# Optimization experiments

Measured on AMD Instinct MI355X. Metric: run time of the kernel, lower is better.

Reference implementation:

```python
import jax, jax.numpy as jnp
import numpy as np

K = 20  # n_neighbors
SLOPE = 0.2

def _act(h):
    return jax.nn.leaky_relu(h, negative_slope=SLOPE)

def _knn_indices(pts):
    # pts: (B, 3, N). Returns (B, N, K) indices of nearest neighbors (by -||xi-xj||^2).
    sq = jnp.sum(pts * pts, axis=1)                      # (B, N)
    inner = jnp.einsum('bcn,bcm->bnm', pts, pts)         # (B, N, N)
    neg_dist = 2.0 * inner - sq[:, :, None] - sq[:, None, :]
    _, idx = jax.lax.top_k(neg_dist, K)                  # (B, N, K)
    return idx

def _gather_neighbors(feats, idx):
    # feats: (B, N, C), idx: (B, N, K) -> (B, N, K, C)
    return jax.vmap(lambda f, i: f[i])(feats, idx)

def setup_inputs() -> dict:
    key = jax.random.key(0)
    ks = jax.random.split(key, 7)
    B, N = 16, 2048
    dims = [64, 64, 128, 256]
    s = 0.05
    inp = {
        'x':  jax.random.normal(ks[0], (B, N, 3), jnp.float32),
        'W0': jax.random.normal(ks[1], (dims[0], 6), jnp.float32) * s,
        'b0': jnp.zeros((dims[0],), jnp.float32),
        'W1': jax.random.normal(ks[2], (dims[1], dims[0]), jnp.float32) * s,
        'b1': jnp.zeros((dims[1],), jnp.float32),
        'W2': jax.random.normal(ks[3], (dims[2], dims[1]), jnp.float32) * s,
        'b2': jnp.zeros((dims[2],), jnp.float32),
        'W3': jax.random.normal(ks[4], (dims[3], dims[2]), jnp.float32) * s,
        'b3': jnp.zeros((dims[3],), jnp.float32),
        'Wf': jax.random.normal(ks[5], (1024, sum(dims)), jnp.float32) * s,
        'bf': jnp.zeros((1024,), jnp.float32),
    }
    return inp

def reference(x, W0, b0, W1, b1, W2, b2, W3, b3, Wf, bf):
    # x: (B, N, 3)
    pts = jnp.swapaxes(x, 1, 2)                          # (B, 3, N)
    idx = _knn_indices(pts)                              # (B, N, K)

    # get_graph_features: edge feats = [neighbor - center, center], (B, N, K, 6)
    neigh = _gather_neighbors(x, idx)                    # (B, N, K, 3)
    center = jnp.broadcast_to(x[:, :, None, :], neigh.shape)
    edge = jnp.concatenate([neigh - center, center], axis=-1)

    # EdgeConv (1x1 conv) + act, then max over neighbors
    h = _act(jnp.einsum('bnkc,oc->bnko', edge, W0) + b0)  # (B, N, K, 64)
    feat = jnp.max(h, axis=2)                             # (B, N, 64)

    xs = [feat]
    for W, b in ((W1, b1), (W2, b2), (W3, b3)):
        # graph max pooling over the fixed kNN graph
        pooled = jnp.max(_gather_neighbors(feat, idx), axis=2)  # (B, N, C)
        feat = _act(jnp.einsum('bnc,oc->bno', pooled, W) + b)
        xs.append(feat)

    cat = jnp.concatenate(xs, axis=-1)                    # (B, N, 512)
    out = _act(jnp.einsum('bnc,oc->bno', cat, Wf) + bf)   # (B, N, 1024)
    return jnp.max(out, axis=1)                           # (B, 1024)
```

## Files before the change

### kernel.cpp

```cpp
#include <hip/hip_runtime.h>

#define K_NN 20
#define NEG_INF (-__builtin_inff())

constexpr int BB   = 16;
constexpr int NN   = 2048;
constexpr int CATC = 512;
constexpr int ROW_G = BB * NN;

typedef short bf16x8 __attribute__((ext_vector_type(8)));
typedef float f32x4  __attribute__((ext_vector_type(4)));

__device__ __forceinline__ unsigned short f2bf_rn(float f) {
  unsigned int u = __float_as_uint(f);
  unsigned int r = u + 0x7FFFu + ((u >> 16) & 1u);
  return (unsigned short)(r >> 16);
}
__device__ __forceinline__ float bf2f(unsigned short h) {
  return __uint_as_float((unsigned int)h << 16);
}
__device__ __forceinline__ void split_store(float v, unsigned short* ph, unsigned short* pl) {
  const unsigned short h = f2bf_rn(v);
  *ph = h;
  *pl = f2bf_rn(v - bf2f(h));
}
__device__ __forceinline__ float join_hl(unsigned short h, unsigned short l) {
  return bf2f(h) + bf2f(l);
}

__device__ __forceinline__ int mbcnt(unsigned long long mask) {
  return __builtin_amdgcn_mbcnt_hi((unsigned int)(mask >> 32),
         __builtin_amdgcn_mbcnt_lo((unsigned int)mask, 0));
}

#define DECL_VALS(INIT) \
  unsigned int v0=INIT,v1=INIT,v2=INIT,v3=INIT,v4=INIT,v5=INIT,v6=INIT,v7=INIT, \
               v8=INIT,v9=INIT,v10=INIT,v11=INIT,v12=INIT,v13=INIT,v14=INIT,    \
               v15=INIT,v16=INIT,v17=INIT,v18=INIT,v19=INIT;

#define INSERT_VAL(x) do {                         \
    v19 = min(v18, max(v19, (x)));                 \
    v18 = min(v17, max(v18, (x)));                 \
    v17 = min(v16, max(v17, (x)));                 \
    v16 = min(v15, max(v16, (x)));                 \
    v15 = min(v14, max(v15, (x)));                 \
    v14 = min(v13, max(v14, (x)));                 \
    v13 = min(v12, max(v13, (x)));                 \
    v12 = min(v11, max(v12, (x)));                 \
    v11 = min(v10, max(v11, (x)));                 \
    v10 = min(v9,  max(v10, (x)));                 \
    v9  = min(v8,  max(v9,  (x)));                 \
    v8  = min(v7,  max(v8,  (x)));                 \
    v7  = min(v6,  max(v7,  (x)));                 \
    v6  = min(v5,  max(v6,  (x)));                 \
    v5  = min(v4,  max(v5,  (x)));                 \
    v4  = min(v3,  max(v4,  (x)));                 \
    v3  = min(v2,  max(v3,  (x)));                 \
    v2  = min(v1,  max(v2,  (x)));                 \
    v1  = min(v0,  max(v1,  (x)));                 \
    v0  = max(v0, (x));                            \
  } while (0)

__device__ __forceinline__ unsigned int sortable(float d) {
  unsigned int ub = __float_as_uint(d);
  return (ub & 0x80000000u) ? ~ub : (ub | 0x80000000u);
}

__global__ __launch_bounds__(128) void knn_chunk_kernel(const float* __restrict__ x,
                                                        unsigned int* __restrict__ cv) {
  __shared__ float4 cand[256];
  const int bid = blockIdx.x;
  const int ch = bid & 7;
  const int rt = (bid >> 3) & 15;
  const int b  = bid >> 7;
  const float* xb = x + (size_t)b * NN * 3;

  for (int i = threadIdx.x; i < 256; i += 128) {
    const int m = ch * 256 + i;
    const float px = xb[m*3+0], py = xb[m*3+1], pz = xb[m*3+2];
    cand[i] = make_float4(px, py, pz, fmaf(pz, pz, fmaf(py, py, px*px)));
  }
  __syncthreads();

  const int n = rt * 128 + threadIdx.x;
  const float cx = xb[n*3+0], cy = xb[n*3+1], cz = xb[n*3+2];
  const float csq = fmaf(cz, cz, fmaf(cy, cy, cx*cx));

  DECL_VALS(0u)

#pragma unroll 4
  for (int i = 0; i < 256; ++i) {
    const float4 c = cand[i];
    const float inner = fmaf(cz, c.z, fmaf(cy, c.y, cx*c.x));
    const float d = 2.0f * inner - csq - c.w;
    const unsigned int u = sortable(d);
    INSERT_VAL(u);
  }

  const int rowg = b * NN + n;
#define STORE_VAL(i) cv[(size_t)(ch*K_NN + i) * ROW_G + rowg] = v##i;
  STORE_VAL(0) STORE_VAL(1) STORE_VAL(2) STORE_VAL(3) STORE_VAL(4)
  STORE_VAL(5) STORE_VAL(6) STORE_VAL(7) STORE_VAL(8) STORE_VAL(9)
  STORE_VAL(10) STORE_VAL(11) STORE_VAL(12) STORE_VAL(13) STORE_VAL(14)
  STORE_VAL(15) STORE_VAL(16) STORE_VAL(17) STORE_VAL(18) STORE_VAL(19)
#undef STORE_VAL
}

__global__ __launch_bounds__(64) void knn_d20_kernel(const unsigned int* __restrict__ cv,
                                                     unsigned int* __restrict__ d20g) {
  const int r = blockIdx.x * 64 + threadIdx.x;
#define LOAD_VAL(i) unsigned int v##i = cv[(size_t)i * ROW_G + r];
  LOAD_VAL(0) LOAD_VAL(1) LOAD_VAL(2) LOAD_VAL(3) LOAD_VAL(4)
  LOAD_VAL(5) LOAD_VAL(6) LOAD_VAL(7) LOAD_VAL(8) LOAD_VAL(9)
  LOAD_VAL(10) LOAD_VAL(11) LOAD_VAL(12) LOAD_VAL(13) LOAD_VAL(14)
  LOAD_VAL(15) LOAD_VAL(16) LOAD_VAL(17) LOAD_VAL(18) LOAD_VAL(19)
#undef LOAD_VAL
#pragma unroll 4
  for (int i = K_NN; i < 8 * K_NN; ++i)
    INSERT_VAL(cv[(size_t)i * ROW_G + r]);
  d20g[r] = v19;
}

__global__ __launch_bounds__(256) void knn_collect_kernel(const float* __restrict__ x,
    const unsigned int* __restrict__ d20g, int* __restrict__ idx_out) {
  __shared__ float4 cand[NN];
  __shared__ int tie[4][K_NN];
  const int w = threadIdx.x >> 6, lane = threadIdx.x & 63;
  const int r = blockIdx.x * 4 + w;
  const int b = r >> 11;
  const float* xb = x + (size_t)b * NN * 3;

  for (int i = threadIdx.x; i < NN; i += 256) {
    const float px = xb[i*3+0], py = xb[i*3+1], pz = xb[i*3+2];
    cand[i] = make_float4(px, py, pz, fmaf(pz, pz, fmaf(py, py, px*px)));
  }
  __syncthreads();

  const int n = r & (NN - 1);
  const float4 ctr = cand[n];
  const unsigned int d20 = d20g[r];
  int* op = idx_out + (size_t)r * K_NN;
  int cg = 0, ce = 0;

#pragma unroll 4
  for (int k = 0; k < NN / 64; ++k) {
    const int i = k * 64 + lane;
    const float4 c = cand[i];
    const float inner = fmaf(ctr.z, c.z, fmaf(ctr.y, c.y, ctr.x*c.x));
    const float d = 2.0f * inner - ctr.w - c.w;
    const unsigned int u = sortable(d);
    const unsigned long long mb = __ballot(u > d20);
    if (u > d20) op[cg + mbcnt(mb)] = i;
    cg += __popcll(mb);
    const unsigned long long tb = __ballot(u == d20);
    if (tb) {
      if (u == d20) {
        const int pos = ce + mbcnt(tb);
        if (pos < K_NN) tie[w][pos] = i;
      }
      ce += __popcll(tb);
    }
  }
  if (lane == 0)
    for (int j = 0; cg < K_NN; ++j, ++cg) op[cg] = tie[w][j];
}

__global__ __launch_bounds__(256) void edgeconv_kernel(const float* __restrict__ x,
    const int* __restrict__ idx, const float* __restrict__ W0,
    const float* __restrict__ b0, unsigned short* __restrict__ Ahg,
    unsigned short* __restrict__ Alg) {
  const int o  = threadIdx.x & 63;
  const int pt = blockIdx.x * 4 + (threadIdx.x >> 6);
  const int b  = pt >> 11, n = pt & (NN - 1);
  const float* xb = x + (size_t)b * NN * 3;

  const float w0 = W0[o*6+0], w1 = W0[o*6+1], w2 = W0[o*6+2];
  const float w3 = W0[o*6+3], w4 = W0[o*6+4], w5 = W0[o*6+5];
  const float bias = b0[o];
  const float cx = xb[n*3+0], cy = xb[n*3+1], cz = xb[n*3+2];

  const int* ip = idx + (size_t)pt * K_NN;
  float px = 0.f, py = 0.f, pz = 0.f;
  if (o < K_NN) { const int m = ip[o]; px = xb[m*3+0]; py = xb[m*3+1]; pz = xb[m*3+2]; }

  float best = NEG_INF;
#pragma unroll
  for (int k = 0; k < K_NN; ++k) {
    const float ax = __shfl(px, k, 64), ay = __shfl(py, k, 64), az = __shfl(pz, k, 64);
    float h = w0 * (ax - cx);
    h = fmaf(w1, ay - cy, h);
    h = fmaf(w2, az - cz, h);
    h = fmaf(w3, cx, h);
    h = fmaf(w4, cy, h);
    h = fmaf(w5, cz, h);
    h += bias;
    h = (h > 0.f) ? h : 0.2f * h;
    best = fmaxf(best, h);
  }
  split_store(best, &Ahg[(size_t)pt * CATC + o], &Alg[(size_t)pt * CATC + o]);
}

template<int CIN, int COUT, int PTS>
__global__ __launch_bounds__(256) void pool_mlp_kernel(
    unsigned short* __restrict__ Ahg, unsigned short* __restrict__ Alg,
    const int* __restrict__ idx, const float* __restrict__ W,
    const float* __restrict__ bias, int coff_in, int coff_out) {
  __shared__ float pooled[PTS][CIN];
  __shared__ int sidx[PTS][K_NN];
  const int pt0 = blockIdx.x * PTS;

  for (int t = threadIdx.x; t < PTS * K_NN; t += 256)
    sidx[t / K_NN][t % K_NN] = idx[(size_t)pt0 * K_NN + t];
  __syncthreads();

  for (int t = threadIdx.x; t < PTS * CIN; t += 256) {
    const int p = t / CIN, c = t % CIN;
    const int bq = (pt0 + p) >> 11;
    const size_t base = (size_t)bq * NN * CATC + coff_in + c;
    float mv = NEG_INF;
#pragma unroll
    for (int k = 0; k < K_NN; ++k) {
      const size_t a = base + (size_t)sidx[p][k] * CATC;
      mv = fmaxf(mv, join_hl(Ahg[a], Alg[a]));
    }
    pooled[p][c] = mv;
  }
  __syncthreads();

  for (int t = threadIdx.x; t < PTS * COUT; t += 256) {
    const int p = t / COUT, o = t % COUT;
    const float4* pp = (const float4*)&pooled[p][0];
    const float4* wp = (const float4*)(W + (size_t)o * CIN);
    float acc = 0.f;
#pragma unroll
    for (int c4 = 0; c4 < CIN / 4; ++c4) {
      const float4 pv = pp[c4], wv = wp[c4];
      acc = fmaf(pv.x, wv.x, acc);
      acc = fmaf(pv.y, wv.y, acc);
      acc = fmaf(pv.z, wv.z, acc);
      acc = fmaf(pv.w, wv.w, acc);
    }
    float h = acc + bias[o];
    h = (h > 0.f) ? h : 0.2f * h;
    const size_t a = (size_t)(pt0 + p) * CATC + coff_out + o;
    split_store(h, &Ahg[a], &Alg[a]);
  }
}

__global__ __launch_bounds__(256) void wsplit_kernel(const float* __restrict__ Wf,
    unsigned short* __restrict__ Wh, unsigned short* __restrict__ Wl) {
  const int t = blockIdx.x * 256 + threadIdx.x;
  const float4 v = ((const float4*)Wf)[t];
  ushort4 h4, l4;
  h4.x = f2bf_rn(v.x); l4.x = f2bf_rn(v.x - bf2f(h4.x));
  h4.y = f2bf_rn(v.y); l4.y = f2bf_rn(v.y - bf2f(h4.y));
  h4.z = f2bf_rn(v.z); l4.z = f2bf_rn(v.z - bf2f(h4.z));
  h4.w = f2bf_rn(v.w); l4.w = f2bf_rn(v.w - bf2f(h4.w));
  ((ushort4*)Wh)[t] = h4;
  ((ushort4*)Wl)[t] = l4;
}

__global__ __launch_bounds__(256) void final_gemm_mfma(
    const unsigned short* __restrict__ Ahg, const unsigned short* __restrict__ Alg,
    const unsigned short* __restrict__ Whg, const unsigned short* __restrict__ Wlg,
    float* __restrict__ partials) {
  __shared__ __align__(16) unsigned short AhL[128][40];
  __shared__ __align__(16) unsigned short AlL[128][40];
  __shared__ __align__(16) unsigned short WhL[128][40];
  __shared__ __align__(16) unsigned short WlL[128][40];
  __shared__ float smax[2][128];

  const int ot    = blockIdx.x;
  const int chunk = blockIdx.y;
  const int b     = blockIdx.z;
  const int tid   = threadIdx.x;
  const int lane  = tid & 63;
  const int w     = tid >> 6;
  const int wr    = w >> 1;
  const int wc    = w & 1;
  const int fr    = lane & 15;
  const int kg    = lane >> 4;

  const int srow = tid >> 1;
  const int shalf = (tid & 1) * 16;
  const size_t arow = ((size_t)(b * NN) + (size_t)chunk * 128 + srow) * CATC;
  const size_t wrow = ((size_t)ot * 128 + srow) * CATC;

  f32x4 acc[4][4];
#pragma unroll
  for (int i = 0; i < 4; ++i)
#pragma unroll
    for (int j = 0; j < 4; ++j) acc[i][j] = (f32x4){0.f, 0.f, 0.f, 0.f};

  for (int kt = 0; kt < 16; ++kt) {
    const int k0 = kt * 32;
    const uint4 a0 = *(const uint4*)(Ahg + arow + k0 + shalf);
    const uint4 a1 = *(const uint4*)(Ahg + arow + k0 + shalf + 8);
    const uint4 a2 = *(const uint4*)(Alg + arow + k0 + shalf);
    const uint4 a3 = *(const uint4*)(Alg + arow + k0 + shalf + 8);
    const uint4 w0 = *(const uint4*)(Whg + wrow + k0 + shalf);
    const uint4 w1 = *(const uint4*)(Whg + wrow + k0 + shalf + 8);
    const uint4 w2 = *(const uint4*)(Wlg + wrow + k0 + shalf);
    const uint4 w3 = *(const uint4*)(Wlg + wrow + k0 + shalf + 8);
    __syncthreads();
    *(uint4*)&AhL[srow][shalf]     = a0;
    *(uint4*)&AhL[srow][shalf + 8] = a1;
    *(uint4*)&AlL[srow][shalf]     = a2;
    *(uint4*)&AlL[srow][shalf + 8] = a3;
    *(uint4*)&WhL[srow][shalf]     = w0;
    *(uint4*)&WhL[srow][shalf + 8] = w1;
    *(uint4*)&WlL[srow][shalf]     = w2;
    *(uint4*)&WlL[srow][shalf + 8] = w3;
    __syncthreads();

    bf16x8 ahf[4], alf[4], whf[4], wlf[4];
#pragma unroll
    for (int i = 0; i < 4; ++i) {
      ahf[i] = *(const bf16x8*)&AhL[wr * 64 + i * 16 + fr][kg * 8];
      alf[i] = *(const bf16x8*)&AlL[wr * 64 + i * 16 + fr][kg * 8];
    }
#pragma unroll
    for (int j = 0; j < 4; ++j) {
      whf[j] = *(const bf16x8*)&WhL[wc * 64 + j * 16 + fr][kg * 8];
      wlf[j] = *(const bf16x8*)&WlL[wc * 64 + j * 16 + fr][kg * 8];
    }

#pragma unroll
    for (int i = 0; i < 4; ++i)
#pragma unroll
      for (int j = 0; j < 4; ++j) {
        acc[i][j] = __builtin_amdgcn_mfma_f32_16x16x32_bf16(ahf[i], whf[j], acc[i][j], 0, 0, 0);
        acc[i][j] = __builtin_amdgcn_mfma_f32_16x16x32_bf16(ahf[i], wlf[j], acc[i][j], 0, 0, 0);
        acc[i][j] = __builtin_amdgcn_mfma_f32_16x16x32_bf16(alf[i], whf[j], acc[i][j], 0, 0, 0);
      }
  }

#pragma unroll
  for (int j = 0; j < 4; ++j) {
    float mj = NEG_INF;
#pragma unroll
    for (int i = 0; i < 4; ++i) {
      mj = fmaxf(mj, fmaxf(fmaxf(acc[i][j][0], acc[i][j][1]),
                           fmaxf(acc[i][j][2], acc[i][j][3])));
    }
    mj = fmaxf(mj, __shfl_xor(mj, 16, 64));
    mj = fmaxf(mj, __shfl_xor(mj, 32, 64));
    if (lane < 16) smax[wr][wc * 64 + j * 16 + fr] = mj;
  }
  __syncthreads();
  if (tid < 128) {
    const float m = fmaxf(smax[0][tid], smax[1][tid]);
    partials[((size_t)(b * 16 + chunk)) * 1024 + (size_t)ot * 128 + tid] = m;
  }
}

__global__ __launch_bounds__(256) void final_reduce_kernel(const float* __restrict__ partials,
    const float* __restrict__ bf, float* __restrict__ out) {
  const int t = blockIdx.x * 256 + threadIdx.x;
  const int b = t >> 10, o = t & 1023;
  float m = NEG_INF;
#pragma unroll
  for (int c = 0; c < 16; ++c)
    m = fmaxf(m, partials[((size_t)(b * 16 + c)) * 1024 + o]);
  float h = m + bf[o];
  out[t] = (h > 0.f) ? h : 0.2f * h;
}

extern "C" void kernel_launch(void* const* d_in, const int* in_sizes, int n_in,
                              void* d_out, int out_size, void* d_ws, size_t ws_size,
                              hipStream_t stream) {
  (void)in_sizes; (void)n_in; (void)out_size; (void)ws_size;
  const float* x  = (const float*)d_in[0];
  const float* W0 = (const float*)d_in[1];
  const float* b0 = (const float*)d_in[2];
  const float* W1 = (const float*)d_in[3];
  const float* b1 = (const float*)d_in[4];
  const float* W2 = (const float*)d_in[5];
  const float* b2 = (const float*)d_in[6];
  const float* W3 = (const float*)d_in[7];
  const float* b3 = (const float*)d_in[8];
  const float* Wf = (const float*)d_in[9];
  const float* bf = (const float*)d_in[10];
  float* out = (float*)d_out;

  char* ws = (char*)d_ws;
  int* idx_ws = (int*)ws;
  unsigned short* Wh = (unsigned short*)ws;
  unsigned short* Wl = (unsigned short*)(ws + 1048576);
  unsigned int* cv = (unsigned int*)(ws + 2621440);
  unsigned int* d20g = (unsigned int*)(ws + 23592960);
  unsigned short* Ah = (unsigned short*)(ws + 2621440);
  unsigned short* Al = (unsigned short*)(ws + 36175872);
  float* partials = (float*)(ws + 69730304);

  knn_chunk_kernel<<<BB * 16 * 8, 128, 0, stream>>>(x, cv);
  knn_d20_kernel<<<ROW_G / 64, 64, 0, stream>>>(cv, d20g);
  knn_collect_kernel<<<ROW_G / 4, 256, 0, stream>>>(x, d20g, idx_ws);
  edgeconv_kernel<<<ROW_G / 4, 256, 0, stream>>>(x, idx_ws, W0, b0, Ah, Al);
  pool_mlp_kernel<64, 64, 16><<<ROW_G / 16, 256, 0, stream>>>(Ah, Al, idx_ws, W1, b1, 0, 64);
  pool_mlp_kernel<64, 128, 8><<<ROW_G / 8, 256, 0, stream>>>(Ah, Al, idx_ws, W2, b2, 64, 128);
  pool_mlp_kernel<128, 256, 8><<<ROW_G / 8, 256, 0, stream>>>(Ah, Al, idx_ws, W3, b3, 128, 256);
  wsplit_kernel<<<512, 256, 0, stream>>>(Wf, Wh, Wl);
  final_gemm_mfma<<<dim3(8, 16, BB), 256, 0, stream>>>(Ah, Al, Wh, Wl, partials);
  final_reduce_kernel<<<BB * 1024 / 256, 256, 0, stream>>>(partials, bf, out);
}
```

Before: 534.2 us.

## Prefetch next K tile into registers and remap final GEMM blocks for XCD locality

```diff
diff --git a/kernel.cpp b/kernel.cpp
--- a/kernel.cpp
+++ b/kernel.cpp
@@ -268,11 +268,16 @@
   __shared__ __align__(16) unsigned short AlL[128][40];
   __shared__ __align__(16) unsigned short WhL[128][40];
   __shared__ __align__(16) unsigned short WlL[128][40];
-  __shared__ float smax[2][128];
-
-  const int ot    = blockIdx.x;
-  const int chunk = blockIdx.y;
-  const int b     = blockIdx.z;
+
+  const int L     = blockIdx.x + (blockIdx.y << 3) + (blockIdx.z << 7);
+  const int xcd   = L & 7;
+  const int q     = L >> 3;
+  const int ot    = q & 7;
+  const int s     = q >> 3;
+  const int p     = (s << 3) | xcd;
+  const int chunk = p & 15;
+  const int b     = p >> 4;
+
   const int tid   = threadIdx.x;
   const int lane  = tid & 63;
   const int w     = tid >> 6;
@@ -292,25 +297,36 @@
 #pragma unroll
     for (int j = 0; j < 4; ++j) acc[i][j] = (f32x4){0.f, 0.f, 0.f, 0.f};
 
+  uint4 ra0 = *(const uint4*)(Ahg + arow + shalf);
+  uint4 ra1 = *(const uint4*)(Ahg + arow + shalf + 8);
+  uint4 ra2 = *(const uint4*)(Alg + arow + shalf);
+  uint4 ra3 = *(const uint4*)(Alg + arow + shalf + 8);
+  uint4 rw0 = *(const uint4*)(Whg + wrow + shalf);
+  uint4 rw1 = *(const uint4*)(Whg + wrow + shalf + 8);
+  uint4 rw2 = *(const uint4*)(Wlg + wrow + shalf);
+  uint4 rw3 = *(const uint4*)(Wlg + wrow + shalf + 8);
+
   for (int kt = 0; kt < 16; ++kt) {
-    const int k0 = kt * 32;
-    const uint4 a0 = *(const uint4*)(Ahg + arow + k0 + shalf);
-    const uint4 a1 = *(const uint4*)(Ahg + arow + k0 + shalf + 8);
-    const uint4 a2 = *(const uint4*)(Alg + arow + k0 + shalf);
-    const uint4 a3 = *(const uint4*)(Alg + arow + k0 + shalf + 8);
-    const uint4 w0 = *(const uint4*)(Whg + wrow + k0 + shalf);
-    const uint4 w1 = *(const uint4*)(Whg + wrow + k0 + shalf + 8);
-    const uint4 w2 = *(const uint4*)(Wlg + wrow + k0 + shalf);
-    const uint4 w3 = *(const uint4*)(Wlg + wrow + k0 + shalf + 8);
     __syncthreads();
-    *(uint4*)&AhL[srow][shalf]     = a0;
-    *(uint4*)&AhL[srow][shalf + 8] = a1;
-    *(uint4*)&AlL[srow][shalf]     = a2;
-    *(uint4*)&AlL[srow][shalf + 8] = a3;
-    *(uint4*)&WhL[srow][shalf]     = w0;
-    *(uint4*)&WhL[srow][shalf + 8] = w1;
-    *(uint4*)&WlL[srow][shalf]     = w2;
-    *(uint4*)&WlL[srow][shalf + 8] = w3;
+    *(uint4*)&AhL[srow][shalf]     = ra0;
+    *(uint4*)&AhL[srow][shalf + 8] = ra1;
+    *(uint4*)&AlL[srow][shalf]     = ra2;
+    *(uint4*)&AlL[srow][shalf + 8] = ra3;
+    *(uint4*)&WhL[srow][shalf]     = rw0;
+    *(uint4*)&WhL[srow][shalf + 8] = rw1;
+    *(uint4*)&WlL[srow][shalf]     = rw2;
+    *(uint4*)&WlL[srow][shalf + 8] = rw3;
+    if (kt < 15) {
+      const int k0 = (kt + 1) * 32;
+      ra0 = *(const uint4*)(Ahg + arow + k0 + shalf);
+      ra1 = *(const uint4*)(Ahg + arow + k0 + shalf + 8);
+      ra2 = *(const uint4*)(Alg + arow + k0 + shalf);
+      ra3 = *(const uint4*)(Alg + arow + k0 + shalf + 8);
+      rw0 = *(const uint4*)(Whg + wrow + k0 + shalf);
+      rw1 = *(const uint4*)(Whg + wrow + k0 + shalf + 8);
+      rw2 = *(const uint4*)(Wlg + wrow + k0 + shalf);
+      rw3 = *(const uint4*)(Wlg + wrow + k0 + shalf + 8);
+    }
     __syncthreads();
 
     bf16x8 ahf[4], alf[4], whf[4], wlf[4];
@@ -335,6 +351,8 @@
       }
   }
 
+  __syncthreads();
+  float* smax = (float*)&AhL[0][0];
 #pragma unroll
   for (int j = 0; j < 4; ++j) {
     float mj = NEG_INF;
@@ -345,11 +363,11 @@
     }
     mj = fmaxf(mj, __shfl_xor(mj, 16, 64));
     mj = fmaxf(mj, __shfl_xor(mj, 32, 64));
-    if (lane < 16) smax[wr][wc * 64 + j * 16 + fr] = mj;
+    if (lane < 16) smax[wr * 128 + wc * 64 + j * 16 + fr] = mj;
   }
   __syncthreads();
   if (tid < 128) {
-    const float m = fmaxf(smax[0][tid], smax[1][tid]);
+    const float m = fmaxf(smax[tid], smax[128 + tid]);
     partials[((size_t)(b * 16 + chunk)) * 1024 + (size_t)ot * 128 + tid] = m;
   }
 }
```

Result: faster. 517.3 us (-3.2%).
